# Kernel tuning notes

Measured on AMD Instinct MI355X. Metric: run time of the kernel, lower is better.

The kernel has to match this reference:

```python
import jax, jax.numpy as jnp
import numpy as np

B, D, E, H, K = 8192, 1024, 8, 4096, 2

def setup_inputs() -> dict:
    key = jax.random.key(0)
    ks = jax.random.split(key, 7)
    s_in = 1.0 / np.sqrt(D)
    s_hid = 1.0 / np.sqrt(H)
    return {
        "z":  jax.random.normal(ks[0], (B, D), dtype=jnp.float32),
        "Wg": jax.random.uniform(ks[1], (D, E), jnp.float32, -s_in, s_in),
        "bg": jnp.zeros((E,), jnp.float32),
        "W1": jax.random.uniform(ks[2], (E, D, H), jnp.float32, -s_in, s_in),
        "b1": jax.random.uniform(ks[3], (E, H), jnp.float32, -s_in, s_in),
        "W2": jax.random.uniform(ks[4], (E, H, D), jnp.float32, -s_hid, s_hid),
        "b2": jax.random.uniform(ks[5], (E, D), jnp.float32, -s_hid, s_hid),
    }

def reference(z, Wg, bg, W1, b1, W2, b2):
    # gate: softmax over experts, then keep only top-k weights (no renorm,
    # matching the original which sums topw * expert(z))
    w = jax.nn.softmax(z @ Wg + bg, axis=-1)            # [B, E]
    topw, idx = jax.lax.top_k(w, K)                      # [B, K] each
    wmask = jnp.zeros_like(w).at[jnp.arange(B)[:, None], idx].set(topw)  # [B, E]
    # dense all-expert MLP, then weighted combine (same math as per-token loop)
    h = jax.nn.relu(jnp.einsum('bd,edh->beh', z, W1) + b1)   # [B, E, H]
    y = jnp.einsum('beh,ehd->bed', h, W2) + b2               # [B, E, D]
    out = jnp.einsum('be,bed->bd', wmask, y)                 # [B, D]
    return out
```

## Files before the change

### kernel.cpp

```cpp
#include <hip/hip_runtime.h>
#include <hip/hip_bf16.h>
#include <cstdint>
#include <cstddef>

#define BTOK  8192
#define DIM   1024
#define NEXP  8
#define NHID  4096
#define HHALF 2048
#define GATE_TOK 64

typedef __bf16 bf16x8 __attribute__((ext_vector_type(8)));
typedef float  floatx4 __attribute__((ext_vector_type(4)));

#define O_COUNTS 0
#define O_BASE   256
#define O_TOKB   1024
#define O_TOKW   (O_TOKB + (size_t)NEXP*BTOK*4)
#define O_CE     (O_TOKW + (size_t)NEXP*BTOK*4)
#define O_CP     (O_CE + (size_t)2*BTOK*4)
#define O_CW     (O_CP + (size_t)2*BTOK*4)
#define O_ZBF    (O_CW + (size_t)2*BTOK*4)
#define O_W1T    (O_ZBF + (size_t)BTOK*DIM*2)
#define O_W2T    (O_W1T + (size_t)NEXP*DIM*NHID*2)
#define O_HBUF   (O_W2T + (size_t)NEXP*DIM*NHID*2)
#define WS_BASE  (O_HBUF + (size_t)2*BTOK*HHALF*2)
#define O_YBUF   WS_BASE
#define WS_FULL  (O_YBUF + (size_t)2*BTOK*DIM*4)

__device__ __forceinline__ void gload_lds16(const void* g, void* l) {
  __builtin_amdgcn_global_load_lds(
      (const __attribute__((address_space(1))) void*)g,
      (__attribute__((address_space(3))) void*)l, 16, 0, 0);
}

__device__ __forceinline__ ushort f2bf(float x) {
  return __builtin_bit_cast(ushort, __float2bfloat16(x));
}

__global__ void k_zcnt(int* __restrict__ counts) {
  if (threadIdx.x < NEXP) counts[threadIdx.x] = 0;
}

__global__ void k_zout(float* __restrict__ out) {
  int i = blockIdx.x * blockDim.x + threadIdx.x;
  float4 z4 = {0.f, 0.f, 0.f, 0.f};
  float4* o = (float4*)out;
  int n = BTOK * DIM / 4;
  for (int j = i; j < n; j += gridDim.x * blockDim.x) o[j] = z4;
}

__global__ __launch_bounds__(256) void k_transpose(
    const float* __restrict__ src, __hip_bfloat16* __restrict__ dst, int R, int C) {
  __shared__ float tile[32][33];
  int zz = blockIdx.z;
  const float* s = src + (size_t)zz * R * C;
  __hip_bfloat16* d = dst + (size_t)zz * R * C;
  int c0 = blockIdx.x * 32, r0 = blockIdx.y * 32;
  int tx = threadIdx.x & 31, ty = threadIdx.x >> 5;
#pragma unroll
  for (int i = ty; i < 32; i += 8)
    tile[i][tx] = s[(size_t)(r0 + i) * C + c0 + tx];
  __syncthreads();
#pragma unroll
  for (int i = ty; i < 32; i += 8)
    d[(size_t)(c0 + i) * R + r0 + tx] = __float2bfloat16(tile[tx][i]);
}

__global__ __launch_bounds__(256) void k_gate(
    const float* __restrict__ z, const float* __restrict__ Wg,
    const float* __restrict__ bg, int* __restrict__ counts,
    int* __restrict__ tokb, float* __restrict__ tokw,
    int* __restrict__ ce, int* __restrict__ cp, float* __restrict__ cw,
    __hip_bfloat16* __restrict__ zbf) {
  __shared__ float wgT[NEXP * DIM];
  __shared__ int   le[2 * GATE_TOK];
  __shared__ float lw[2 * GATE_TOK];
  __shared__ int   lr[2 * GATE_TOK];
  __shared__ int   lcnt[NEXP];
  __shared__ int   gbase[NEXP];

  int tid = threadIdx.x;
  if (tid < NEXP) lcnt[tid] = 0;
#pragma unroll
  for (int e = 0; e < NEXP; e++)
    for (int d = tid; d < DIM; d += 256)
      wgT[e * DIM + d] = Wg[d * NEXP + e];
  __syncthreads();

  int lane = tid & 63;
  int wv = tid >> 6;
  int b0 = blockIdx.x * GATE_TOK;

  for (int t = 0; t < 16; t++) {
    int lt = wv * 16 + t;
    int b = b0 + lt;
    const float4* zr4 = (const float4*)(z + (size_t)b * DIM);
    float4 zv[4];
#pragma unroll
    for (int i = 0; i < 4; i++) zv[i] = zr4[lane + 64 * i];
    ushort4* zb4 = (ushort4*)((ushort*)zbf + (size_t)b * DIM);
#pragma unroll
    for (int i = 0; i < 4; i++) {
      ushort4 u;
      u.x = f2bf(zv[i].x); u.y = f2bf(zv[i].y);
      u.z = f2bf(zv[i].z); u.w = f2bf(zv[i].w);
      zb4[lane + 64 * i] = u;
    }
    float acc[NEXP];
#pragma unroll
    for (int e = 0; e < NEXP; e++) acc[e] = 0.f;
#pragma unroll
    for (int e = 0; e < NEXP; e++) {
      const float4* wg4 = (const float4*)(wgT + e * DIM);
#pragma unroll
      for (int i = 0; i < 4; i++) {
        float4 w4 = wg4[lane + 64 * i];
        acc[e] += zv[i].x * w4.x + zv[i].y * w4.y + zv[i].z * w4.z + zv[i].w * w4.w;
      }
    }
#pragma unroll
    for (int off = 32; off > 0; off >>= 1) {
#pragma unroll
      for (int e = 0; e < NEXP; e++) acc[e] += __shfl_down(acc[e], off);
    }
    if (lane == 0) {
      float mx = -1e30f;
#pragma unroll
      for (int e = 0; e < NEXP; e++) { acc[e] += bg[e]; mx = fmaxf(mx, acc[e]); }
      float s = 0.f;
#pragma unroll
      for (int e = 0; e < NEXP; e++) { acc[e] = expf(acc[e] - mx); s += acc[e]; }
      float inv = 1.f / s;
      int i1 = -1, i2 = -1; float v1 = -1.f, v2 = -1.f;
#pragma unroll
      for (int e = 0; e < NEXP; e++) {
        float w = acc[e] * inv;
        if (w > v1) { v2 = v1; i2 = i1; v1 = w; i1 = e; }
        else if (w > v2) { v2 = w; i2 = e; }
      }
      le[2 * lt] = i1;     lw[2 * lt] = v1;
      le[2 * lt + 1] = i2; lw[2 * lt + 1] = v2;
    }
  }
  __syncthreads();
  if (tid < 2 * GATE_TOK) lr[tid] = atomicAdd(&lcnt[le[tid]], 1);
  __syncthreads();
  if (tid < NEXP) gbase[tid] = atomicAdd(&counts[tid], lcnt[tid]);
  __syncthreads();
  if (tid < 2 * GATE_TOK) {
    int e = le[tid];
    int p = gbase[e] + lr[tid];
    int b = b0 + (tid >> 1);
    int slot = tid & 1;
    tokb[e * BTOK + p] = b;
    tokw[e * BTOK + p] = lw[tid];
    ce[2 * b + slot] = e;
    cp[2 * b + slot] = p;
    cw[2 * b + slot] = lw[tid];
  }
}

__global__ void k_base(const int* __restrict__ counts, int* __restrict__ base) {
  if (threadIdx.x == 0 && blockIdx.x == 0) {
    int s = 0;
    for (int e = 0; e < NEXP; e++) { base[e] = s; s += counts[e]; }
  }
}

__global__ __launch_bounds__(256, 3) void k_gemm1(
    const __hip_bfloat16* __restrict__ zbf, const __hip_bfloat16* __restrict__ w1t,
    const float* __restrict__ b1, const int* __restrict__ counts,
    const int* __restrict__ base, const int* __restrict__ tokb,
    __hip_bfloat16* __restrict__ hbuf, int hbase) {
  int e = blockIdx.z;
  int cnt = counts[e];
  int n0 = blockIdx.y * 128;
  int gb = base[e];

  __shared__ __align__(16) ushort sA[128 * 64];
  __shared__ __align__(16) ushort sB[128 * 64];

  int tid = threadIdx.x;
  int lane = tid & 63;
  int wv = tid >> 6;
  int wmoff = (wv >> 1) * 64;
  int wnoff = (wv & 1) * 64;
  int lrow = lane & 15;
  int quad = lane >> 4;
  int subrow = lane >> 3;
  int clog = (lane & 7) ^ subrow;

  const ushort* zb = (const ushort*)zbf;
  const ushort* w1 = (const ushort*)w1t;
  const ushort* gB[4];
#pragma unroll
  for (int s4 = 0; s4 < 4; s4++) {
    int r = wv * 8 + subrow + s4 * 32;
    gB[s4] = w1 + (size_t)(e * NHID + hbase + n0 + r) * DIM + clog * 8;
  }

  for (int mt = blockIdx.x; mt * 128 < cnt; mt += gridDim.x) {
    int m0 = mt * 128;
    const ushort* gA[4];
#pragma unroll
    for (int s4 = 0; s4 < 4; s4++) {
      int r = wv * 8 + subrow + s4 * 32;
      int m = m0 + r; if (m >= cnt) m = cnt - 1;
      gA[s4] = zb + (size_t)tokb[e * BTOK + m] * DIM + clog * 8;
    }

    floatx4 acc[4][4];
#pragma unroll
    for (int i = 0; i < 4; i++)
#pragma unroll
      for (int j = 0; j < 4; j++) { floatx4 zf = {0.f,0.f,0.f,0.f}; acc[i][j] = zf; }

    for (int k0 = 0; k0 < DIM; k0 += 64) {
#pragma unroll
      for (int s4 = 0; s4 < 4; s4++) {
        int ldsrow = wv * 8 + s4 * 32;
        gload_lds16(gA[s4] + k0, sA + ldsrow * 64);
        gload_lds16(gB[s4] + k0, sB + ldsrow * 64);
      }
      __syncthreads();
#pragma unroll
      for (int kk = 0; kk < 2; kk++) {
        bf16x8 af[4], bfr[4];
#pragma unroll
        for (int i = 0; i < 4; i++) {
          int row = wmoff + i * 16 + lrow;
          int pc = (kk * 4 + quad) ^ (lrow & 7);
          uint4 t = *(const uint4*)(sA + row * 64 + pc * 8);
          af[i] = __builtin_bit_cast(bf16x8, t);
        }
#pragma unroll
        for (int j = 0; j < 4; j++) {
          int row = wnoff + j * 16 + lrow;
          int pc = (kk * 4 + quad) ^ (lrow & 7);
          uint4 t = *(const uint4*)(sB + row * 64 + pc * 8);
          bfr[j] = __builtin_bit_cast(bf16x8, t);
        }
#pragma unroll
        for (int i = 0; i < 4; i++)
#pragma unroll
          for (int j = 0; j < 4; j++)
            acc[i][j] = __builtin_amdgcn_mfma_f32_16x16x32_bf16(af[i], bfr[j], acc[i][j], 0, 0, 0);
      }
      __syncthreads();
    }

#pragma unroll
    for (int i = 0; i < 4; i++) {
      int mloc = wmoff + i * 16 + quad * 4;
#pragma unroll
      for (int r = 0; r < 4; r++) {
        int m = m0 + mloc + r;
        if (m < cnt) {
#pragma unroll
          for (int j = 0; j < 4; j++) {
            int n = n0 + wnoff + j * 16 + lrow;
            float v = acc[i][j][r] + b1[e * NHID + hbase + n];
            v = fmaxf(v, 0.f);
            hbuf[(size_t)(gb + m) * HHALF + n] = __float2bfloat16(v);
          }
        }
      }
    }
  }
}

__global__ __launch_bounds__(256, 3) void k_gemm2(
    const __hip_bfloat16* __restrict__ hbuf, const __hip_bfloat16* __restrict__ w2t,
    const float* __restrict__ b2, const int* __restrict__ counts,
    const int* __restrict__ base, const int* __restrict__ tokb,
    const float* __restrict__ tokw, float* __restrict__ out,
    float* __restrict__ ybuf, int hbase, int pass) {
  int e = blockIdx.z;
  int cnt = counts[e];
  int n0 = blockIdx.y * 128;
  int gb = base[e];

  __shared__ __align__(16) ushort sA[128 * 64];
  __shared__ __align__(16) ushort sB[128 * 64];

  int tid = threadIdx.x;
  int lane = tid & 63;
  int wv = tid >> 6;
  int wmoff = (wv >> 1) * 64;
  int wnoff = (wv & 1) * 64;
  int lrow = lane & 15;
  int quad = lane >> 4;
  int subrow = lane >> 3;
  int clog = (lane & 7) ^ subrow;

  const ushort* hb = (const ushort*)hbuf;
  const ushort* w2 = (const ushort*)w2t;
  const ushort* gB[4];
#pragma unroll
  for (int s4 = 0; s4 < 4; s4++) {
    int r = wv * 8 + subrow + s4 * 32;
    gB[s4] = w2 + (size_t)(e * DIM + n0 + r) * NHID + hbase + clog * 8;
  }

  for (int mt = blockIdx.x; mt * 128 < cnt; mt += gridDim.x) {
    int m0 = mt * 128;
    const ushort* gA[4];
#pragma unroll
    for (int s4 = 0; s4 < 4; s4++) {
      int r = wv * 8 + subrow + s4 * 32;
      int mm = m0 + r; if (mm >= cnt) mm = cnt - 1;
      gA[s4] = hb + (size_t)(gb + mm) * HHALF + clog * 8;
    }

    floatx4 acc[4][4];
#pragma unroll
    for (int i = 0; i < 4; i++)
#pragma unroll
      for (int j = 0; j < 4; j++) { floatx4 zf = {0.f,0.f,0.f,0.f}; acc[i][j] = zf; }

    for (int k0 = 0; k0 < HHALF; k0 += 64) {
#pragma unroll
      for (int s4 = 0; s4 < 4; s4++) {
        int ldsrow = wv * 8 + s4 * 32;
        gload_lds16(gA[s4] + k0, sA + ldsrow * 64);
        gload_lds16(gB[s4] + k0, sB + ldsrow * 64);
      }
      __syncthreads();
#pragma unroll
      for (int kk = 0; kk < 2; kk++) {
        bf16x8 af[4], bfr[4];
#pragma unroll
        for (int i = 0; i < 4; i++) {
          int row = wmoff + i * 16 + lrow;
          int pc = (kk * 4 + quad) ^ (lrow & 7);
          uint4 t = *(const uint4*)(sA + row * 64 + pc * 8);
          af[i] = __builtin_bit_cast(bf16x8, t);
        }
#pragma unroll
        for (int j = 0; j < 4; j++) {
          int row = wnoff + j * 16 + lrow;
          int pc = (kk * 4 + quad) ^ (lrow & 7);
          uint4 t = *(const uint4*)(sB + row * 64 + pc * 8);
          bfr[j] = __builtin_bit_cast(bf16x8, t);
        }
#pragma unroll
        for (int i = 0; i < 4; i++)
#pragma unroll
          for (int j = 0; j < 4; j++)
            acc[i][j] = __builtin_amdgcn_mfma_f32_16x16x32_bf16(af[i], bfr[j], acc[i][j], 0, 0, 0);
      }
      __syncthreads();
    }

#pragma unroll
    for (int i = 0; i < 4; i++) {
      int mloc = wmoff + i * 16 + quad * 4;
#pragma unroll
      for (int r = 0; r < 4; r++) {
        int m = m0 + mloc + r;
        if (m < cnt) {
          if (ybuf) {
            float* yr = ybuf + (size_t)(gb + m) * DIM;
#pragma unroll
            for (int j = 0; j < 4; j++) {
              int n = n0 + wnoff + j * 16 + lrow;
              float v = acc[i][j][r];
              if (pass == 0) yr[n] = v;
              else           yr[n] += v + b2[e * DIM + n];
            }
          } else {
            int t  = tokb[e * BTOK + m];
            float w = tokw[e * BTOK + m];
#pragma unroll
            for (int j = 0; j < 4; j++) {
              int n = n0 + wnoff + j * 16 + lrow;
              float v = acc[i][j][r] + (pass ? b2[e * DIM + n] : 0.f);
              atomicAdd(&out[(size_t)t * DIM + n], w * v);
            }
          }
        }
      }
    }
  }
}

__global__ __launch_bounds__(256) void k_combine(
    const float* __restrict__ ybuf, const int* __restrict__ base,
    const int* __restrict__ ce, const int* __restrict__ cp,
    const float* __restrict__ cw, float* __restrict__ out) {
  int b = blockIdx.x;
  int n = threadIdx.x * 4;
  int e1 = ce[2 * b], e2 = ce[2 * b + 1];
  int s1 = base[e1] + cp[2 * b];
  int s2 = base[e2] + cp[2 * b + 1];
  float w1 = cw[2 * b], w2 = cw[2 * b + 1];
  float4 a = *(const float4*)(ybuf + (size_t)s1 * DIM + n);
  float4 c = *(const float4*)(ybuf + (size_t)s2 * DIM + n);
  float4 o;
  o.x = w1 * a.x + w2 * c.x;
  o.y = w1 * a.y + w2 * c.y;
  o.z = w1 * a.z + w2 * c.z;
  o.w = w1 * a.w + w2 * c.w;
  *(float4*)(out + (size_t)b * DIM + n) = o;
}

extern "C" void kernel_launch(void* const* d_in, const int* in_sizes, int n_in,
                              void* d_out, int out_size, void* d_ws, size_t ws_size,
                              hipStream_t stream) {
  const float* z  = (const float*)d_in[0];
  const float* Wg = (const float*)d_in[1];
  const float* bg = (const float*)d_in[2];
  const float* W1 = (const float*)d_in[3];
  const float* b1 = (const float*)d_in[4];
  const float* W2 = (const float*)d_in[5];
  const float* b2 = (const float*)d_in[6];
  float* out = (float*)d_out;
  char* ws = (char*)d_ws;
  if (ws_size < WS_BASE) return;
  bool use_ybuf = ws_size >= WS_FULL;

  int*   counts = (int*)(ws + O_COUNTS);
  int*   base   = (int*)(ws + O_BASE);
  int*   tokb   = (int*)(ws + O_TOKB);
  float* tokw   = (float*)(ws + O_TOKW);
  int*   ce     = (int*)(ws + O_CE);
  int*   cp     = (int*)(ws + O_CP);
  float* cw     = (float*)(ws + O_CW);
  __hip_bfloat16* zbf  = (__hip_bfloat16*)(ws + O_ZBF);
  __hip_bfloat16* w1t  = (__hip_bfloat16*)(ws + O_W1T);
  __hip_bfloat16* w2t  = (__hip_bfloat16*)(ws + O_W2T);
  __hip_bfloat16* hbuf = (__hip_bfloat16*)(ws + O_HBUF);
  float* ybuf = use_ybuf ? (float*)(ws + O_YBUF) : nullptr;

  k_zcnt<<<1, 64, 0, stream>>>(counts);
  if (!use_ybuf) k_zout<<<512, 256, 0, stream>>>(out);
  k_transpose<<<dim3(NHID / 32, DIM / 32, NEXP), 256, 0, stream>>>(W1, w1t, DIM, NHID);
  k_transpose<<<dim3(DIM / 32, NHID / 32, NEXP), 256, 0, stream>>>(W2, w2t, NHID, DIM);
  k_gate<<<BTOK / GATE_TOK, 256, 0, stream>>>(z, Wg, bg, counts, tokb, tokw, ce, cp, cw, zbf);
  k_base<<<1, 64, 0, stream>>>(counts, base);
  for (int half = 0; half < 2; half++) {
    k_gemm1<<<dim3(16, HHALF / 128, NEXP), 256, 0, stream>>>(
        zbf, w1t, b1, counts, base, tokb, hbuf, half * HHALF);
    k_gemm2<<<dim3(16, DIM / 128, NEXP), 256, 0, stream>>>(
        hbuf, w2t, b2, counts, base, tokb, tokw, out, ybuf, half * HHALF, half);
  }
  if (use_ybuf)
    k_combine<<<BTOK, 256, 0, stream>>>(ybuf, base, ce, cp, cw, out);
}
```

Before: 937.9 us.

## Use 256x256 tiles with 4-stage async LDS pipeline in expert GEMMs

Both expert GEMMs move from 128x128 tiles with a single-buffered K=64 loop to 256x256 tiles over 512 threads, with a 4-slot K=32 LDS ring buffer and prefetch three stages ahead. Barriers now use explicit vmcnt/lgkmcnt waits, and the MFMA block is wrapped in s_setprio so loads overlap compute. This targets global-load latency and the low arithmetic intensity of the smaller tiles. The costs are higher register pressure (32 accumulators per lane), more LDS per block, and fewer blocks per expert, which could leave CUs idle when an expert has few tokens.

```diff
diff --git a/kernel.cpp b/kernel.cpp
--- a/kernel.cpp
+++ b/kernel.cpp
@@ -9,6 +9,7 @@
 #define NHID  4096
 #define HHALF 2048
 #define GATE_TOK 64
+#define BK 32
 
 typedef __bf16 bf16x8 __attribute__((ext_vector_type(8)));
 typedef float  floatx4 __attribute__((ext_vector_type(4)));
@@ -168,101 +169,136 @@
   }
 }
 
-__global__ __launch_bounds__(256, 3) void k_gemm1(
+
+#define STAGE(t_) do {                                                          \
+    int s_ = (t_) & 3;                                                          \
+    _Pragma("unroll")                                                           \
+    for (int q_ = 0; q_ < 2; q_++) {                                            \
+      gload_lds16(srcA[q_] + (t_) * BK, &lds[s_][0][(q_ * 128 + wv * 16) * BK]);\
+      gload_lds16(srcB[q_] + (t_) * BK, &lds[s_][1][(q_ * 128 + wv * 16) * BK]);\
+    }                                                                           \
+  } while (0)
+
+#define BAR_A(vm) do {                                                          \
+    asm volatile("s_waitcnt vmcnt(" #vm ")" ::: "memory");                      \
+    __builtin_amdgcn_s_barrier();                                               \
+    asm volatile("" ::: "memory");                                              \
+  } while (0)
+
+#define BAR_B() do {                                                            \
+    asm volatile("s_waitcnt lgkmcnt(0)" ::: "memory");                          \
+    __builtin_amdgcn_s_barrier();                                               \
+    asm volatile("" ::: "memory");                                              \
+  } while (0)
+
+#define MFMA_TILE(slot_) do {                                                   \
+    const ushort* As_ = &lds[(slot_)][0][0];                                    \
+    const ushort* Bs_ = &lds[(slot_)][1][0];                                    \
+    bf16x8 afr[8], bfr[4];                                                      \
+    _Pragma("unroll")                                                           \
+    for (int j_ = 0; j_ < 4; j_++)                                              \
+      bfr[j_] = __builtin_bit_cast(bf16x8,                                      \
+          *(const uint4*)(Bs_ + (wn * 64 + j_ * 16 + lrow) * BK + cswz));       \
+    _Pragma("unroll")                                                           \
+    for (int i_ = 0; i_ < 8; i_++)                                              \
+      afr[i_] = __builtin_bit_cast(bf16x8,                                      \
+          *(const uint4*)(As_ + (wm * 128 + i_ * 16 + lrow) * BK + cswz));      \
+    __builtin_amdgcn_s_setprio(1);                                              \
+    _Pragma("unroll")                                                           \
+    for (int i_ = 0; i_ < 8; i_++)                                              \
+      _Pragma("unroll")                                                         \
+      for (int j_ = 0; j_ < 4; j_++)                                            \
+        acc[i_][j_] = __builtin_amdgcn_mfma_f32_16x16x32_bf16(                  \
+            afr[i_], bfr[j_], acc[i_][j_], 0, 0, 0);                            \
+    __builtin_amdgcn_s_setprio(0);                                              \
+  } while (0)
+
+__global__ __launch_bounds__(512, 2) void k_gemm1(
     const __hip_bfloat16* __restrict__ zbf, const __hip_bfloat16* __restrict__ w1t,
     const float* __restrict__ b1, const int* __restrict__ counts,
     const int* __restrict__ base, const int* __restrict__ tokb,
     __hip_bfloat16* __restrict__ hbuf, int hbase) {
   int e = blockIdx.z;
   int cnt = counts[e];
-  int n0 = blockIdx.y * 128;
+  if (cnt == 0) return;
+  int n0 = blockIdx.y * 256;
   int gb = base[e];
 
-  __shared__ __align__(16) ushort sA[128 * 64];
-  __shared__ __align__(16) ushort sB[128 * 64];
+  __shared__ __align__(16) ushort lds[4][2][256 * BK];
 
   int tid = threadIdx.x;
   int lane = tid & 63;
   int wv = tid >> 6;
-  int wmoff = (wv >> 1) * 64;
-  int wnoff = (wv & 1) * 64;
+  int wm = wv >> 2;
+  int wn = wv & 3;
   int lrow = lane & 15;
   int quad = lane >> 4;
-  int subrow = lane >> 3;
-  int clog = (lane & 7) ^ subrow;
+  int cswz = (quad ^ ((lrow >> 1) & 3)) * 8;
+
+  int srow = wv * 16 + (lane >> 2);
+  int schunk = lane & 3;
 
   const ushort* zb = (const ushort*)zbf;
   const ushort* w1 = (const ushort*)w1t;
-  const ushort* gB[4];
-#pragma unroll
-  for (int s4 = 0; s4 < 4; s4++) {
-    int r = wv * 8 + subrow + s4 * 32;
-    gB[s4] = w1 + (size_t)(e * NHID + hbase + n0 + r) * DIM + clog * 8;
-  }
-
-  for (int mt = blockIdx.x; mt * 128 < cnt; mt += gridDim.x) {
-    int m0 = mt * 128;
-    const ushort* gA[4];
-#pragma unroll
-    for (int s4 = 0; s4 < 4; s4++) {
-      int r = wv * 8 + subrow + s4 * 32;
+
+  const ushort* srcB[2];
+#pragma unroll
+  for (int q = 0; q < 2; q++) {
+    int r = q * 128 + srow;
+    srcB[q] = w1 + (size_t)(e * NHID + hbase + n0 + r) * DIM
+                 + (size_t)((schunk ^ ((r >> 1) & 3)) * 8);
+  }
+
+  const int NT = DIM / BK;
+
+  for (int mt = blockIdx.x; mt * 256 < cnt; mt += gridDim.x) {
+    int m0 = mt * 256;
+    const ushort* srcA[2];
+#pragma unroll
+    for (int q = 0; q < 2; q++) {
+      int r = q * 128 + srow;
       int m = m0 + r; if (m >= cnt) m = cnt - 1;
-      gA[s4] = zb + (size_t)tokb[e * BTOK + m] * DIM + clog * 8;
-    }
-
-    floatx4 acc[4][4];
-#pragma unroll
-    for (int i = 0; i < 4; i++)
+      srcA[q] = zb + (size_t)tokb[e * BTOK + m] * DIM
+                   + (size_t)((schunk ^ ((r >> 1) & 3)) * 8);
+    }
+
+#pragma unroll
+    for (int t = 0; t < 3; t++) STAGE(t);
+
+    floatx4 acc[8][4];
+#pragma unroll
+    for (int i = 0; i < 8; i++)
 #pragma unroll
       for (int j = 0; j < 4; j++) { floatx4 zf = {0.f,0.f,0.f,0.f}; acc[i][j] = zf; }
 
-    for (int k0 = 0; k0 < DIM; k0 += 64) {
-#pragma unroll
-      for (int s4 = 0; s4 < 4; s4++) {
-        int ldsrow = wv * 8 + s4 * 32;
-        gload_lds16(gA[s4] + k0, sA + ldsrow * 64);
-        gload_lds16(gB[s4] + k0, sB + ldsrow * 64);
-      }
-      __syncthreads();
-#pragma unroll
-      for (int kk = 0; kk < 2; kk++) {
-        bf16x8 af[4], bfr[4];
-#pragma unroll
-        for (int i = 0; i < 4; i++) {
-          int row = wmoff + i * 16 + lrow;
-          int pc = (kk * 4 + quad) ^ (lrow & 7);
-          uint4 t = *(const uint4*)(sA + row * 64 + pc * 8);
-          af[i] = __builtin_bit_cast(bf16x8, t);
-        }
-#pragma unroll
-        for (int j = 0; j < 4; j++) {
-          int row = wnoff + j * 16 + lrow;
-          int pc = (kk * 4 + quad) ^ (lrow & 7);
-          uint4 t = *(const uint4*)(sB + row * 64 + pc * 8);
-          bfr[j] = __builtin_bit_cast(bf16x8, t);
-        }
-#pragma unroll
-        for (int i = 0; i < 4; i++)
-#pragma unroll
-          for (int j = 0; j < 4; j++)
-            acc[i][j] = __builtin_amdgcn_mfma_f32_16x16x32_bf16(af[i], bfr[j], acc[i][j], 0, 0, 0);
-      }
-      __syncthreads();
-    }
-
-#pragma unroll
-    for (int i = 0; i < 4; i++) {
-      int mloc = wmoff + i * 16 + quad * 4;
+#pragma unroll 1
+    for (int t = 0; t < NT - 3; t++) {
+      STAGE(t + 3);
+      BAR_A(12);
+      MFMA_TILE(t & 3);
+      BAR_B();
+    }
+    BAR_A(8);  MFMA_TILE((NT - 3) & 3);  BAR_B();
+    BAR_A(4);  MFMA_TILE((NT - 2) & 3);  BAR_B();
+    BAR_A(0);  MFMA_TILE((NT - 1) & 3);  BAR_B();
+
+    float bias[4];
+#pragma unroll
+    for (int j = 0; j < 4; j++)
+      bias[j] = b1[e * NHID + hbase + n0 + wn * 64 + j * 16 + lrow];
+    ushort* hp = (ushort*)hbuf;
+#pragma unroll
+    for (int i = 0; i < 8; i++) {
+      int mloc = wm * 128 + i * 16 + quad * 4;
 #pragma unroll
       for (int r = 0; r < 4; r++) {
         int m = m0 + mloc + r;
         if (m < cnt) {
+          ushort* hr = hp + (size_t)(gb + m) * HHALF;
 #pragma unroll
           for (int j = 0; j < 4; j++) {
-            int n = n0 + wnoff + j * 16 + lrow;
-            float v = acc[i][j][r] + b1[e * NHID + hbase + n];
-            v = fmaxf(v, 0.f);
-            hbuf[(size_t)(gb + m) * HHALF + n] = __float2bfloat16(v);
+            float v = fmaxf(acc[i][j][r] + bias[j], 0.f);
+            hr[n0 + wn * 64 + j * 16 + lrow] = f2bf(v);
           }
         }
       }
@@ -270,7 +306,7 @@
   }
 }
 
-__global__ __launch_bounds__(256, 3) void k_gemm2(
+__global__ __launch_bounds__(512, 2) void k_gemm2(
     const __hip_bfloat16* __restrict__ hbuf, const __hip_bfloat16* __restrict__ w2t,
     const float* __restrict__ b2, const int* __restrict__ counts,
     const int* __restrict__ base, const int* __restrict__ tokb,
@@ -278,105 +314,105 @@
     float* __restrict__ ybuf, int hbase, int pass) {
   int e = blockIdx.z;
   int cnt = counts[e];
-  int n0 = blockIdx.y * 128;
+  if (cnt == 0) return;
+  int n0 = blockIdx.y * 256;
   int gb = base[e];
 
-  __shared__ __align__(16) ushort sA[128 * 64];
-  __shared__ __align__(16) ushort sB[128 * 64];
+  __shared__ __align__(16) ushort lds[4][2][256 * BK];
 
   int tid = threadIdx.x;
   int lane = tid & 63;
   int wv = tid >> 6;
-  int wmoff = (wv >> 1) * 64;
-  int wnoff = (wv & 1) * 64;
+  int wm = wv >> 2;
+  int wn = wv & 3;
   int lrow = lane & 15;
   int quad = lane >> 4;
-  int subrow = lane >> 3;
-  int clog = (lane & 7) ^ subrow;
+  int cswz = (quad ^ ((lrow >> 1) & 3)) * 8;
+
+  int srow = wv * 16 + (lane >> 2);
+  int schunk = lane & 3;
 
   const ushort* hb = (const ushort*)hbuf;
   const ushort* w2 = (const ushort*)w2t;
-  const ushort* gB[4];
-#pragma unroll
-  for (int s4 = 0; s4 < 4; s4++) {
-    int r = wv * 8 + subrow + s4 * 32;
-    gB[s4] = w2 + (size_t)(e * DIM + n0 + r) * NHID + hbase + clog * 8;
-  }
-
-  for (int mt = blockIdx.x; mt * 128 < cnt; mt += gridDim.x) {
-    int m0 = mt * 128;
-    const ushort* gA[4];
-#pragma unroll
-    for (int s4 = 0; s4 < 4; s4++) {
-      int r = wv * 8 + subrow + s4 * 32;
-      int mm = m0 + r; if (mm >= cnt) mm = cnt - 1;
-      gA[s4] = hb + (size_t)(gb + mm) * HHALF + clog * 8;
-    }
-
-    floatx4 acc[4][4];
-#pragma unroll
-    for (int i = 0; i < 4; i++)
+
+  const ushort* srcB[2];
+#pragma unroll
+  for (int q = 0; q < 2; q++) {
+    int r = q * 128 + srow;
+    srcB[q] = w2 + (size_t)(e * DIM + n0 + r) * NHID + hbase
+                 + (size_t)((schunk ^ ((r >> 1) & 3)) * 8);
+  }
+
+  const int NT = HHALF / BK;
+
+  for (int mt = blockIdx.x; mt * 256 < cnt; mt += gridDim.x) {
+    int m0 = mt * 256;
+    const ushort* srcA[2];
+#pragma unroll
+    for (int q = 0; q < 2; q++) {
+      int r = q * 128 + srow;
+      int m = m0 + r; if (m >= cnt) m = cnt - 1;
+      srcA[q] = hb + (size_t)(gb + m) * HHALF
+                   + (size_t)((schunk ^ ((r >> 1) & 3)) * 8);
+    }
+
+#pragma unroll
+    for (int t = 0; t < 3; t++) STAGE(t);
+
+    floatx4 acc[8][4];
+#pragma unroll
+    for (int i = 0; i < 8; i++)
 #pragma unroll
       for (int j = 0; j < 4; j++) { floatx4 zf = {0.f,0.f,0.f,0.f}; acc[i][j] = zf; }
 
-    for (int k0 = 0; k0 < HHALF; k0 += 64) {
-#pragma unroll
-      for (int s4 = 0; s4 < 4; s4++) {
-        int ldsrow = wv * 8 + s4 * 32;
-        gload_lds16(gA[s4] + k0, sA + ldsrow * 64);
-        gload_lds16(gB[s4] + k0, sB + ldsrow * 64);
+#pragma unroll 1
+    for (int t = 0; t < NT - 3; t++) {
+      STAGE(t + 3);
+      BAR_A(12);
+      MFMA_TILE(t & 3);
+      BAR_B();
+    }
+    BAR_A(8);  MFMA_TILE((NT - 3) & 3);  BAR_B();
+    BAR_A(4);  MFMA_TILE((NT - 2) & 3);  BAR_B();
+    BAR_A(0);  MFMA_TILE((NT - 1) & 3);  BAR_B();
+
+    if (ybuf) {
+      float bias[4];
+#pragma unroll
+      for (int j = 0; j < 4; j++)
+        bias[j] = pass ? b2[e * DIM + n0 + wn * 64 + j * 16 + lrow] : 0.f;
+#pragma unroll
+      for (int i = 0; i < 8; i++) {
+        int mloc = wm * 128 + i * 16 + quad * 4;
+#pragma unroll
+        for (int r = 0; r < 4; r++) {
+          int m = m0 + mloc + r;
+          if (m < cnt) {
+            float* yr = ybuf + (size_t)(gb + m) * DIM;
+#pragma unroll
+            for (int j = 0; j < 4; j++) {
+              int n = n0 + wn * 64 + j * 16 + lrow;
+              if (pass == 0) yr[n] = acc[i][j][r];
+              else           yr[n] += acc[i][j][r] + bias[j];
+            }
+          }
+        }
       }
-      __syncthreads();
-#pragma unroll
-      for (int kk = 0; kk < 2; kk++) {
-        bf16x8 af[4], bfr[4];
-#pragma unroll
-        for (int i = 0; i < 4; i++) {
-          int row = wmoff + i * 16 + lrow;
-          int pc = (kk * 4 + quad) ^ (lrow & 7);
-          uint4 t = *(const uint4*)(sA + row * 64 + pc * 8);
-          af[i] = __builtin_bit_cast(bf16x8, t);
-        }
-#pragma unroll
-        for (int j = 0; j < 4; j++) {
-          int row = wnoff + j * 16 + lrow;
-          int pc = (kk * 4 + quad) ^ (lrow & 7);
-          uint4 t = *(const uint4*)(sB + row * 64 + pc * 8);
-          bfr[j] = __builtin_bit_cast(bf16x8, t);
-        }
-#pragma unroll
-        for (int i = 0; i < 4; i++)
-#pragma unroll
-          for (int j = 0; j < 4; j++)
-            acc[i][j] = __builtin_amdgcn_mfma_f32_16x16x32_bf16(af[i], bfr[j], acc[i][j], 0, 0, 0);
-      }
-      __syncthreads();
-    }
-
-#pragma unroll
-    for (int i = 0; i < 4; i++) {
-      int mloc = wmoff + i * 16 + quad * 4;
-#pragma unroll
-      for (int r = 0; r < 4; r++) {
-        int m = m0 + mloc + r;
-        if (m < cnt) {
-          if (ybuf) {
-            float* yr = ybuf + (size_t)(gb + m) * DIM;
+    } else {
+#pragma unroll
+      for (int i = 0; i < 8; i++) {
+        int mloc = wm * 128 + i * 16 + quad * 4;
+#pragma unroll
+        for (int r = 0; r < 4; r++) {
+          int m = m0 + mloc + r;
+          if (m < cnt) {
+            int tk  = tokb[e * BTOK + m];
+            float w = tokw[e * BTOK + m];
 #pragma unroll
             for (int j = 0; j < 4; j++) {
-              int n = n0 + wnoff + j * 16 + lrow;
-              float v = acc[i][j][r];
-              if (pass == 0) yr[n] = v;
-              else           yr[n] += v + b2[e * DIM + n];
-            }
-          } else {
-            int t  = tokb[e * BTOK + m];
-            float w = tokw[e * BTOK + m];
-#pragma unroll
-            for (int j = 0; j < 4; j++) {
-              int n = n0 + wnoff + j * 16 + lrow;
+              int n = n0 + wn * 64 + j * 16 + lrow;
               float v = acc[i][j][r] + (pass ? b2[e * DIM + n] : 0.f);
-              atomicAdd(&out[(size_t)t * DIM + n], w * v);
+              atomicAdd(&out[(size_t)tk * DIM + n], w * v);
             }
           }
         }
@@ -440,9 +476,9 @@
   k_gate<<<BTOK / GATE_TOK, 256, 0, stream>>>(z, Wg, bg, counts, tokb, tokw, ce, cp, cw, zbf);
   k_base<<<1, 64, 0, stream>>>(counts, base);
   for (int half = 0; half < 2; half++) {
-    k_gemm1<<<dim3(16, HHALF / 128, NEXP), 256, 0, stream>>>(
+    k_gemm1<<<dim3(8, HHALF / 256, NEXP), 512, 0, stream>>>(
         zbf, w1t, b1, counts, base, tokb, hbuf, half * HHALF);
-    k_gemm2<<<dim3(16, DIM / 128, NEXP), 256, 0, stream>>>(
+    k_gemm2<<<dim3(8, DIM / 256, NEXP), 512, 0, stream>>>(
         hbuf, w2t, b2, counts, base, tokb, tokw, out, ybuf, half * HHALF, half);
   }
   if (use_ybuf)
```

After: 1.010 ms. +7.6%, slower.
